# Kernel tuning notes

Measured on AMD Instinct MI355X. Metric: run time of the kernel, lower is better.

Reference implementation:

```python
import jax, jax.numpy as jnp
import numpy as np
from jax import lax

EPSILON = 0.05      # sinkhorn entropic regularization (module init arg)
N_SINKHORN = 100    # fixed iteration count (POT default numItermax=1000 w/ early stop 1e-9)


def setup_inputs() -> dict:
    key = jax.random.key(0)
    k1, k2, k3 = jax.random.split(key, 3)
    B, D = 2048, 1024
    audio_emb = jax.random.normal(k1, (B, D), dtype=jnp.float32)
    text_emb = jax.random.normal(k2, (B, D), dtype=jnp.float32)
    # learned metric L (set via set_L); PSD so diag(L) > 0 and sqrt is real
    A = jax.random.normal(k3, (D, D), dtype=jnp.float32)
    L = (A @ A.T) / jnp.float32(D)
    return {"audio_emb": audio_emb, "text_emb": text_emb, "L": L}


def reference(audio_emb, text_emb, L):
    B = audio_emb.shape[0]
    M = jnp.nan_to_num(L)
    # SVD is computed in the original (reg term), but the final loss discards it
    s = jnp.linalg.svd(M, compute_uv=False)
    _reg = jnp.sum(s)  # unused in returned loss (original: loss = wloss)

    # einsum('ijk,ikj,kk->ij') only reads diag(M):
    # M_dist[i,j] = sum_k diag(M)[k] * (audio[j,k] - text[i,k])^2
    w = jnp.diagonal(M)  # [D]
    aw = jnp.einsum('jd,d->j', audio_emb * audio_emb, w)        # [B]
    tw = jnp.einsum('id,d->i', text_emb * text_emb, w)          # [B]
    cross = jnp.einsum('id,jd->ij', text_emb * w, audio_emb)    # [B,B]
    M_dist = tw[:, None] + aw[None, :] - 2.0 * cross
    M_dist = jnp.sqrt(jnp.maximum(M_dist, 0.0))
    M_dist = M_dist / jnp.max(M_dist)

    # Sinkhorn-Knopp (ot.sinkhorn, method='sinkhorn')
    a = jnp.ones((B,), dtype=M_dist.dtype) / B
    b = jnp.ones((B,), dtype=M_dist.dtype) / B
    K = jnp.exp(-M_dist / EPSILON)  # [B,B]

    def step(uv, _):
        u, v = uv
        v = b / (K.T @ u)
        u = a / (K @ v)
        return (u, v), None

    u0 = jnp.ones((B,), dtype=M_dist.dtype) / B
    v0 = jnp.ones((B,), dtype=M_dist.dtype) / B
    (u, v), _ = lax.scan(step, (u0, v0), None, length=N_SINKHORN)
    # pi = diag(u) K diag(v); pi_hat = eye(B)/B -> only diag(pi) matters
    pi_diag = u * jnp.diagonal(K) * v  # [B]
    wloss = -jnp.sum(jnp.log(pi_diag)) / B
    return wloss
```

## Files before the change

### kernel.cpp

```cpp
#include <hip/hip_runtime.h>
#include <hip/hip_fp16.h>
#include <math.h>

#define NB 2048
#define ND 1024
#define EPS 0.05f
#define NITER 100
#define SBLK 256

typedef float f32x4 __attribute__((ext_vector_type(4)));
typedef float f32x2 __attribute__((ext_vector_type(2)));
typedef short s16x8 __attribute__((ext_vector_type(8)));
typedef unsigned short u16x4 __attribute__((ext_vector_type(4)));
union Uh { f32x4 f; __half2 h[4]; };

__global__ void prep_k(const float* __restrict__ L, float* __restrict__ w,
                       float* __restrict__ u, float* __restrict__ v,
                       unsigned* __restrict__ maxbits, unsigned* __restrict__ flags) {
    int gtid = blockIdx.x * 256 + threadIdx.x;
    if (gtid < ND) {
        float x = L[(size_t)gtid * (ND + 1)];
        if (x != x) x = 0.f;
        else if (fabsf(x) == INFINITY) x = (x > 0.f) ? 3.4028235e38f : -3.4028235e38f;
        w[gtid] = x;
    }
    u[gtid] = 1.0f / NB;
    v[gtid] = 1.0f / NB;
    if (gtid == 0) *maxbits = 0u;
    if (gtid < 1024) flags[gtid] = 0u;
}

__global__ __launch_bounds__(256) void rows_k(const float* __restrict__ audio,
                                              const float* __restrict__ text,
                                              const float* __restrict__ w,
                                              float* __restrict__ aw, float* __restrict__ tw) {
    int r = blockIdx.x, tid = threadIdx.x;
    float4 wv = *(const float4*)&w[tid * 4];
    float4 a4 = *(const float4*)&audio[(size_t)r * ND + tid * 4];
    float4 t4 = *(const float4*)&text[(size_t)r * ND + tid * 4];
    float sa = a4.x * a4.x * wv.x + a4.y * a4.y * wv.y + a4.z * a4.z * wv.z + a4.w * a4.w * wv.w;
    float st = t4.x * t4.x * wv.x + t4.y * t4.y * wv.y + t4.z * t4.z * wv.z + t4.w * t4.w * wv.w;
    #pragma unroll
    for (int off = 32; off; off >>= 1) {
        sa += __shfl_down(sa, off, 64);
        st += __shfl_down(st, off, 64);
    }
    __shared__ float red[8];
    if ((tid & 63) == 0) { red[tid >> 6] = sa; red[4 + (tid >> 6)] = st; }
    __syncthreads();
    if (tid == 0) {
        aw[r] = red[0] + red[1] + red[2] + red[3];
        tw[r] = red[4] + red[5] + red[6] + red[7];
    }
}

__device__ __forceinline__ unsigned short f2bf(float x) {
    unsigned uu = __float_as_uint(x);
    return (unsigned short)((uu + 0x7FFFu + ((uu >> 16) & 1u)) >> 16);
}

__global__ __launch_bounds__(256) void gemm_mdist(
        const float* __restrict__ Tm, const float* __restrict__ Am,
        const float* __restrict__ wd, const float* __restrict__ tw, const float* __restrict__ aw,
        __half* __restrict__ Md, __half* __restrict__ MdT,
        float* __restrict__ diagMd, unsigned* __restrict__ maxbits) {
    __shared__ __align__(16) unsigned char smem[38912];
    float* wl = (float*)(smem + 34816);
    const int t = threadIdx.x;
    const int row0 = blockIdx.y * 128, col0 = blockIdx.x * 128;
    *(f32x4*)&wl[t * 4] = *(const f32x4*)&wd[t * 4];
    const int wv = t >> 6;
    const int wr = wv >> 1, wc = wv & 1;
    const int l = t & 63, lr = l & 15, kg = l >> 4;
    const int trow = t >> 4, tk4 = t & 15;
    const int px = (((tk4 >> 1) ^ (trow & 7)) << 4) + ((tk4 & 1) << 3);
    f32x4 acc[4][4];
    #pragma unroll
    for (int m = 0; m < 4; ++m)
        #pragma unroll
        for (int n = 0; n < 4; ++n) acc[m][n] = (f32x4){0.f, 0.f, 0.f, 0.f};
    __syncthreads();
    const float* tp = Tm + (size_t)(row0 + trow) * ND + tk4 * 4;
    const float* ap = Am + (size_t)(col0 + trow) * ND + tk4 * 4;
    for (int k0 = 0; k0 < ND; k0 += 64) {
        f32x4 wv4 = *(const f32x4*)&wl[k0 + tk4 * 4];
        __syncthreads();
        #pragma unroll
        for (int s = 0; s < 8; ++s) {
            f32x4 tv = *(const f32x4*)(tp + (size_t)(s * 16) * ND + k0);
            f32x4 av = *(const f32x4*)(ap + (size_t)(s * 16) * ND + k0);
            tv *= wv4;
            u16x4 tb, ab;
            tb[0] = f2bf(tv[0]); tb[1] = f2bf(tv[1]); tb[2] = f2bf(tv[2]); tb[3] = f2bf(tv[3]);
            ab[0] = f2bf(av[0]); ab[1] = f2bf(av[1]); ab[2] = f2bf(av[2]); ab[3] = f2bf(av[3]);
            const int rb = (s * 16 + trow) * 128 + px;
            *(u16x4*)(smem + rb) = tb;
            *(u16x4*)(smem + 16384 + rb) = ab;
        }
        __syncthreads();
        #pragma unroll
        for (int kk = 0; kk < 2; ++kk) {
            const int sl = (((kk << 2) + kg) ^ (lr & 7)) << 4;
            s16x8 af[4], bfr[4];
            #pragma unroll
            for (int m = 0; m < 4; ++m)
                af[m] = *(const s16x8*)(smem + (wr * 64 + m * 16 + lr) * 128 + sl);
            #pragma unroll
            for (int n = 0; n < 4; ++n)
                bfr[n] = *(const s16x8*)(smem + 16384 + (wc * 64 + n * 16 + lr) * 128 + sl);
            #pragma unroll
            for (int m = 0; m < 4; ++m)
                #pragma unroll
                for (int n = 0; n < 4; ++n)
                    acc[m][n] = __builtin_amdgcn_mfma_f32_16x16x32_bf16(af[m], bfr[n], acc[m][n], 0, 0, 0);
        }
    }
    __syncthreads();
    unsigned short* tr = (unsigned short*)smem;
    unsigned short* mdp = (unsigned short*)Md;
    float lmax = 0.f;
    #pragma unroll
    for (int m = 0; m < 4; ++m) {
        #pragma unroll
        for (int r = 0; r < 4; ++r) {
            const int li = wr * 64 + m * 16 + kg * 4 + r;
            const int i = row0 + li;
            const float twi = tw[i];
            #pragma unroll
            for (int n = 0; n < 4; ++n) {
                const int lj = wc * 64 + n * 16 + lr;
                const int j = col0 + lj;
                float md = twi + aw[j] - 2.0f * acc[m][n][r];
                md = sqrtf(fmaxf(md, 0.f));
                lmax = fmaxf(lmax, md);
                const unsigned short hb = __half_as_ushort(__float2half(md));
                mdp[(size_t)i * NB + j] = hb;
                tr[lj * 136 + li] = hb;
                if (i == j) diagMd[i] = md;
            }
        }
    }
    __syncthreads();
    {
        const int jj = t >> 1, ih = (t & 1) * 64;
        unsigned short* dst = (unsigned short*)MdT + (size_t)(col0 + jj) * NB + row0 + ih;
        #pragma unroll
        for (int x = 0; x < 8; ++x)
            *(s16x8*)(dst + x * 8) = *(const s16x8*)&tr[jj * 136 + ih + x * 8];
    }
    #pragma unroll
    for (int off = 32; off; off >>= 1) lmax = fmaxf(lmax, __shfl_down(lmax, off, 64));
    float* red = (float*)(smem + 34816);
    if (l == 0) red[t >> 6] = lmax;
    __syncthreads();
    if (t == 0) {
        float m2 = fmaxf(fmaxf(red[0], red[1]), fmaxf(red[2], red[3]));
        atomicMax(maxbits, __float_as_uint(m2));
    }
}

__device__ __forceinline__ void wait_phase(const unsigned* __restrict__ flags, int l,
                                           unsigned ph) {
    const unsigned* p = flags + (l << 2);
    for (;;) {
        unsigned f0, f1, f2, f3;
        asm volatile("global_load_dword %0, %4, off sc0 sc1\n\t"
                     "global_load_dword %1, %5, off sc0 sc1\n\t"
                     "global_load_dword %2, %6, off sc0 sc1\n\t"
                     "global_load_dword %3, %7, off sc0 sc1\n\t"
                     "s_waitcnt vmcnt(0)"
                     : "=&v"(f0), "=&v"(f1), "=&v"(f2), "=&v"(f3)
                     : "v"(p), "v"(p + 256), "v"(p + 512), "v"(p + 768) : "memory");
        if (__all((f0 >= ph) && (f1 >= ph) && (f2 >= ph) && (f3 >= ph))) break;
        __builtin_amdgcn_s_sleep(1);
    }
}

__device__ __forceinline__ void half_step_reg(const f32x4 (&kreg)[2][8],
                                              const float* __restrict__ xin,
                                              float* __restrict__ xout,
                                              int row0, float ab, int l) {
    const float* p0 = xin + (l << 3);
    f32x4 x[8];
    asm volatile("global_load_dwordx4 %0, %8, off sc0 sc1\n\t"
                 "global_load_dwordx4 %1, %9, off sc0 sc1\n\t"
                 "global_load_dwordx4 %2, %10, off sc0 sc1\n\t"
                 "global_load_dwordx4 %3, %11, off sc0 sc1\n\t"
                 "global_load_dwordx4 %4, %12, off sc0 sc1\n\t"
                 "global_load_dwordx4 %5, %13, off sc0 sc1\n\t"
                 "global_load_dwordx4 %6, %14, off sc0 sc1\n\t"
                 "global_load_dwordx4 %7, %15, off sc0 sc1\n\t"
                 "s_waitcnt vmcnt(0)"
                 : "=&v"(x[0]), "=&v"(x[1]), "=&v"(x[2]), "=&v"(x[3]),
                   "=&v"(x[4]), "=&v"(x[5]), "=&v"(x[6]), "=&v"(x[7])
                 : "v"(p0), "v"(p0 + 4), "v"(p0 + 512), "v"(p0 + 516),
                   "v"(p0 + 1024), "v"(p0 + 1028), "v"(p0 + 1536), "v"(p0 + 1540)
                 : "memory");
    float acc0 = 0.f, acc1 = 0.f;
    #pragma unroll
    for (int j = 0; j < 8; ++j) {
        #pragma unroll
        for (int q = 0; q < 4; ++q) {
            acc0 = fmaf(kreg[0][j][q], x[j][q], acc0);
            acc1 = fmaf(kreg[1][j][q], x[j][q], acc1);
        }
    }
    #pragma unroll
    for (int off = 32; off; off >>= 1) {
        acc0 += __shfl_down(acc0, off, 64);
        acc1 += __shfl_down(acc1, off, 64);
    }
    if (l == 0) {
        f32x2 o;
        o[0] = ab / acc0; o[1] = ab / acc1;
        asm volatile("global_store_dwordx2 %1, %0, off sc0 sc1"
                     :: "v"(o), "v"(xout + row0) : "memory");
    }
    asm volatile("s_waitcnt vmcnt(0)" ::: "memory");
}

__global__ __launch_bounds__(256, 1) void sinkhorn_k(
        const __half* __restrict__ Mdr, const __half* __restrict__ Mdc,
        float* __restrict__ u, float* __restrict__ v,
        const unsigned* __restrict__ maxbits, unsigned* __restrict__ flags) {
    const int tid = threadIdx.x, bid = blockIdx.x;
    const int w = tid >> 6, l = tid & 63;
    const int row0 = (bid << 3) + (w << 1);
    const float ab = 1.0f / NB;
    unsigned* myflag = flags + (bid << 2);
    const float mx = __uint_as_float(*maxbits);
    const float cc = -1.0f / (mx * EPS);
    f32x4 kc[2][8], kr[2][8];
    #pragma unroll
    for (int r = 0; r < 2; ++r) {
        const __half* pc = Mdc + (size_t)(row0 + r) * NB;
        const __half* pr = Mdr + (size_t)(row0 + r) * NB;
        #pragma unroll
        for (int c = 0; c < 4; ++c) {
            const int col = (c << 9) + (l << 3);
            Uh a; a.f = *(const f32x4*)(pc + col);
            Uh b; b.f = *(const f32x4*)(pr + col);
            #pragma unroll
            for (int q = 0; q < 4; ++q) {
                float2 fa = __half22float2(a.h[q]);
                float2 fb = __half22float2(b.h[q]);
                kc[r][2 * c + (q >> 1)][(q & 1) * 2]     = __expf(fa.x * cc);
                kc[r][2 * c + (q >> 1)][(q & 1) * 2 + 1] = __expf(fa.y * cc);
                kr[r][2 * c + (q >> 1)][(q & 1) * 2]     = __expf(fb.x * cc);
                kr[r][2 * c + (q >> 1)][(q & 1) * 2 + 1] = __expf(fb.y * cc);
            }
        }
    }
    for (int it = 0; it < NITER; ++it) {
        wait_phase(flags, l, 2 * it);
        half_step_reg(kc, u, v, row0, ab, l);
        __syncthreads();
        if (tid == 0) {
            unsigned ph = 2 * it + 1;
            asm volatile("global_store_dword %1, %0, off sc0 sc1"
                         :: "v"(ph), "v"(myflag) : "memory");
        }
        wait_phase(flags, l, 2 * it + 1);
        half_step_reg(kr, v, u, row0, ab, l);
        __syncthreads();
        if (tid == 0) {
            unsigned ph = 2 * it + 2;
            asm volatile("global_store_dword %1, %0, off sc0 sc1"
                         :: "v"(ph), "v"(myflag) : "memory");
        }
    }
}

__global__ void loss_k(const float* __restrict__ u, const float* __restrict__ v,
                       const float* __restrict__ diagMd, const unsigned* __restrict__ maxbits,
                       float* __restrict__ out) {
    int tid = threadIdx.x;
    float mx = __uint_as_float(*maxbits);
    float cc = 1.0f / (mx * EPS);
    double s = 0.0;
    for (int i = tid; i < NB; i += 256)
        s += (double)(logf(u[i]) + logf(v[i]) - diagMd[i] * cc);
    #pragma unroll
    for (int off = 32; off; off >>= 1) s += __shfl_down(s, off, 64);
    __shared__ double red[4];
    if ((tid & 63) == 0) red[tid >> 6] = s;
    __syncthreads();
    if (tid == 0)
        out[0] = (float)(-(red[0] + red[1] + red[2] + red[3]) / (double)NB);
}

extern "C" void kernel_launch(void* const* d_in, const int* in_sizes, int n_in,
                              void* d_out, int out_size, void* d_ws, size_t ws_size,
                              hipStream_t stream) {
    const float* audio = (const float*)d_in[0];
    const float* text  = (const float*)d_in[1];
    const float* L     = (const float*)d_in[2];
    char* ws = (char*)d_ws;
    float*    w       = (float*)(ws + 0);
    float*    aw      = (float*)(ws + 4096);
    float*    tw      = (float*)(ws + 12288);
    float*    u       = (float*)(ws + 20480);
    float*    v       = (float*)(ws + 28672);
    float*    diagMd  = (float*)(ws + 36864);
    unsigned* maxbits = (unsigned*)(ws + 45056);
    unsigned* flags   = (unsigned*)(ws + 45312);
    __half*   Md      = (__half*)(ws + 65536);
    __half*   MdT     = (__half*)(ws + 65536 + (size_t)NB * NB * 2);

    prep_k<<<8, 256, 0, stream>>>(L, w, u, v, maxbits, flags);
    rows_k<<<NB, 256, 0, stream>>>(audio, text, w, aw, tw);
    gemm_mdist<<<dim3(16, 16), 256, 0, stream>>>(text, audio, w, tw, aw, Md, MdT, diagMd, maxbits);
    sinkhorn_k<<<SBLK, 256, 0, stream>>>(Md, MdT, u, v, maxbits, flags);
    loss_k<<<1, 256, 0, stream>>>(u, v, diagMd, maxbits, (float*)d_out);
}
```

Measured before the change: 713.8 us.

## Replace flag barrier with epoch-tagged bf16 vector entries in Sinkhorn

Each u/v entry is packed with a 16-bit epoch tag and a bf16 value, so consumers poll the data itself instead of polling separate per-block flags and then reloading the vector. This removes the __syncthreads, the flag store and the extra round trip per half-step, and it makes the column mapping contiguous for each lane. In exchange u/v carry only bf16 precision, which adds rounding error to the Sinkhorn iterations and the loss. Correctness now depends on the tag and value being written atomically within a single 32-bit store.

```diff
diff --git a/kernel.cpp b/kernel.cpp
--- a/kernel.cpp
+++ b/kernel.cpp
@@ -9,14 +9,20 @@
 #define SBLK 256
 
 typedef float f32x4 __attribute__((ext_vector_type(4)));
-typedef float f32x2 __attribute__((ext_vector_type(2)));
+typedef unsigned u32x4 __attribute__((ext_vector_type(4)));
+typedef unsigned u32x2 __attribute__((ext_vector_type(2)));
 typedef short s16x8 __attribute__((ext_vector_type(8)));
 typedef unsigned short u16x4 __attribute__((ext_vector_type(4)));
 union Uh { f32x4 f; __half2 h[4]; };
 
+__device__ __forceinline__ unsigned short f2bf(float x) {
+    unsigned uu = __float_as_uint(x);
+    return (unsigned short)((uu + 0x7FFFu + ((uu >> 16) & 1u)) >> 16);
+}
+
 __global__ void prep_k(const float* __restrict__ L, float* __restrict__ w,
-                       float* __restrict__ u, float* __restrict__ v,
-                       unsigned* __restrict__ maxbits, unsigned* __restrict__ flags) {
+                       unsigned* __restrict__ uP, unsigned* __restrict__ vP,
+                       unsigned* __restrict__ maxbits) {
     int gtid = blockIdx.x * 256 + threadIdx.x;
     if (gtid < ND) {
         float x = L[(size_t)gtid * (ND + 1)];
@@ -24,10 +30,9 @@
         else if (fabsf(x) == INFINITY) x = (x > 0.f) ? 3.4028235e38f : -3.4028235e38f;
         w[gtid] = x;
     }
-    u[gtid] = 1.0f / NB;
-    v[gtid] = 1.0f / NB;
+    uP[gtid] = 0x3A00u;
+    vP[gtid] = 0x3A00u;
     if (gtid == 0) *maxbits = 0u;
-    if (gtid < 1024) flags[gtid] = 0u;
 }
 
 __global__ __launch_bounds__(256) void rows_k(const float* __restrict__ audio,
@@ -52,11 +57,6 @@
         aw[r] = red[0] + red[1] + red[2] + red[3];
         tw[r] = red[4] + red[5] + red[6] + red[7];
     }
-}
-
-__device__ __forceinline__ unsigned short f2bf(float x) {
-    unsigned uu = __float_as_uint(x);
-    return (unsigned short)((uu + 0x7FFFu + ((uu >> 16) & 1u)) >> 16);
 }
 
 __global__ __launch_bounds__(256) void gemm_mdist(
@@ -159,50 +159,50 @@
     }
 }
 
-__device__ __forceinline__ void wait_phase(const unsigned* __restrict__ flags, int l,
-                                           unsigned ph) {
-    const unsigned* p = flags + (l << 2);
-    for (;;) {
-        unsigned f0, f1, f2, f3;
-        asm volatile("global_load_dword %0, %4, off sc0 sc1\n\t"
-                     "global_load_dword %1, %5, off sc0 sc1\n\t"
-                     "global_load_dword %2, %6, off sc0 sc1\n\t"
-                     "global_load_dword %3, %7, off sc0 sc1\n\t"
-                     "s_waitcnt vmcnt(0)"
-                     : "=&v"(f0), "=&v"(f1), "=&v"(f2), "=&v"(f3)
-                     : "v"(p), "v"(p + 256), "v"(p + 512), "v"(p + 768) : "memory");
-        if (__all((f0 >= ph) && (f1 >= ph) && (f2 >= ph) && (f3 >= ph))) break;
+#define LOAD8(p0) asm volatile( \
+        "global_load_dwordx4 %0, %8, off sc0 sc1\n\t" \
+        "global_load_dwordx4 %1, %8, off offset:16 sc0 sc1\n\t" \
+        "global_load_dwordx4 %2, %8, off offset:32 sc0 sc1\n\t" \
+        "global_load_dwordx4 %3, %8, off offset:48 sc0 sc1\n\t" \
+        "global_load_dwordx4 %4, %8, off offset:64 sc0 sc1\n\t" \
+        "global_load_dwordx4 %5, %8, off offset:80 sc0 sc1\n\t" \
+        "global_load_dwordx4 %6, %8, off offset:96 sc0 sc1\n\t" \
+        "global_load_dwordx4 %7, %8, off offset:112 sc0 sc1\n\t" \
+        "s_waitcnt vmcnt(0)" \
+        : "=&v"(d0), "=&v"(d1), "=&v"(d2), "=&v"(d3), \
+          "=&v"(d4), "=&v"(d5), "=&v"(d6), "=&v"(d7) \
+        : "v"(p0) : "memory")
+
+#define CHK4(dd) ((dd[0] >= phw) && (dd[1] >= phw) && (dd[2] >= phw) && (dd[3] >= phw))
+
+__device__ __forceinline__ void half_step_pair(const f32x4 (&kreg)[2][8],
+                                               const unsigned* __restrict__ xin,
+                                               unsigned* __restrict__ xout,
+                                               int row0, float ab, int l,
+                                               unsigned ph, unsigned epout) {
+    const unsigned phw = ph << 16;
+    const unsigned* p0 = xin + (l << 5);
+    u32x4 d0, d1, d2, d3, d4, d5, d6, d7;
+    LOAD8(p0);
+    bool ok = CHK4(d0) && CHK4(d1) && CHK4(d2) && CHK4(d3) &&
+              CHK4(d4) && CHK4(d5) && CHK4(d6) && CHK4(d7);
+    while (!__all(ok)) {
         __builtin_amdgcn_s_sleep(1);
-    }
-}
-
-__device__ __forceinline__ void half_step_reg(const f32x4 (&kreg)[2][8],
-                                              const float* __restrict__ xin,
-                                              float* __restrict__ xout,
-                                              int row0, float ab, int l) {
-    const float* p0 = xin + (l << 3);
-    f32x4 x[8];
-    asm volatile("global_load_dwordx4 %0, %8, off sc0 sc1\n\t"
-                 "global_load_dwordx4 %1, %9, off sc0 sc1\n\t"
-                 "global_load_dwordx4 %2, %10, off sc0 sc1\n\t"
-                 "global_load_dwordx4 %3, %11, off sc0 sc1\n\t"
-                 "global_load_dwordx4 %4, %12, off sc0 sc1\n\t"
-                 "global_load_dwordx4 %5, %13, off sc0 sc1\n\t"
-                 "global_load_dwordx4 %6, %14, off sc0 sc1\n\t"
-                 "global_load_dwordx4 %7, %15, off sc0 sc1\n\t"
-                 "s_waitcnt vmcnt(0)"
-                 : "=&v"(x[0]), "=&v"(x[1]), "=&v"(x[2]), "=&v"(x[3]),
-                   "=&v"(x[4]), "=&v"(x[5]), "=&v"(x[6]), "=&v"(x[7])
-                 : "v"(p0), "v"(p0 + 4), "v"(p0 + 512), "v"(p0 + 516),
-                   "v"(p0 + 1024), "v"(p0 + 1028), "v"(p0 + 1536), "v"(p0 + 1540)
-                 : "memory");
+        if (!ok) {
+            LOAD8(p0);
+            ok = CHK4(d0) && CHK4(d1) && CHK4(d2) && CHK4(d3) &&
+                 CHK4(d4) && CHK4(d5) && CHK4(d6) && CHK4(d7);
+        }
+    }
+    const u32x4 dd[8] = {d0, d1, d2, d3, d4, d5, d6, d7};
     float acc0 = 0.f, acc1 = 0.f;
     #pragma unroll
     for (int j = 0; j < 8; ++j) {
         #pragma unroll
-        for (int q = 0; q < 4; ++q) {
-            acc0 = fmaf(kreg[0][j][q], x[j][q], acc0);
-            acc1 = fmaf(kreg[1][j][q], x[j][q], acc1);
+        for (int k = 0; k < 4; ++k) {
+            float xv = __uint_as_float(dd[j][k] << 16);
+            acc0 = fmaf(kreg[0][j][k], xv, acc0);
+            acc1 = fmaf(kreg[1][j][k], xv, acc1);
         }
     }
     #pragma unroll
@@ -211,75 +211,63 @@
         acc1 += __shfl_down(acc1, off, 64);
     }
     if (l == 0) {
-        f32x2 o;
-        o[0] = ab / acc0; o[1] = ab / acc1;
+        const unsigned tag = epout << 16;
+        u32x2 o;
+        o[0] = tag | (unsigned)f2bf(ab / acc0);
+        o[1] = tag | (unsigned)f2bf(ab / acc1);
         asm volatile("global_store_dwordx2 %1, %0, off sc0 sc1"
                      :: "v"(o), "v"(xout + row0) : "memory");
     }
-    asm volatile("s_waitcnt vmcnt(0)" ::: "memory");
 }
 
 __global__ __launch_bounds__(256, 1) void sinkhorn_k(
         const __half* __restrict__ Mdr, const __half* __restrict__ Mdc,
-        float* __restrict__ u, float* __restrict__ v,
-        const unsigned* __restrict__ maxbits, unsigned* __restrict__ flags) {
+        unsigned* __restrict__ uP, unsigned* __restrict__ vP,
+        const unsigned* __restrict__ maxbits) {
     const int tid = threadIdx.x, bid = blockIdx.x;
     const int w = tid >> 6, l = tid & 63;
     const int row0 = (bid << 3) + (w << 1);
     const float ab = 1.0f / NB;
-    unsigned* myflag = flags + (bid << 2);
     const float mx = __uint_as_float(*maxbits);
     const float cc = -1.0f / (mx * EPS);
     f32x4 kc[2][8], kr[2][8];
     #pragma unroll
     for (int r = 0; r < 2; ++r) {
-        const __half* pc = Mdc + (size_t)(row0 + r) * NB;
-        const __half* pr = Mdr + (size_t)(row0 + r) * NB;
-        #pragma unroll
-        for (int c = 0; c < 4; ++c) {
-            const int col = (c << 9) + (l << 3);
-            Uh a; a.f = *(const f32x4*)(pc + col);
-            Uh b; b.f = *(const f32x4*)(pr + col);
-            #pragma unroll
-            for (int q = 0; q < 4; ++q) {
-                float2 fa = __half22float2(a.h[q]);
-                float2 fb = __half22float2(b.h[q]);
-                kc[r][2 * c + (q >> 1)][(q & 1) * 2]     = __expf(fa.x * cc);
-                kc[r][2 * c + (q >> 1)][(q & 1) * 2 + 1] = __expf(fa.y * cc);
-                kr[r][2 * c + (q >> 1)][(q & 1) * 2]     = __expf(fb.x * cc);
-                kr[r][2 * c + (q >> 1)][(q & 1) * 2 + 1] = __expf(fb.y * cc);
+        const __half* pc = Mdc + (size_t)(row0 + r) * NB + (l << 5);
+        const __half* pr = Mdr + (size_t)(row0 + r) * NB + (l << 5);
+        #pragma unroll
+        for (int q = 0; q < 4; ++q) {
+            Uh a; a.f = *(const f32x4*)(pc + (q << 3));
+            Uh b; b.f = *(const f32x4*)(pr + (q << 3));
+            #pragma unroll
+            for (int h = 0; h < 4; ++h) {
+                float2 fa = __half22float2(a.h[h]);
+                float2 fb = __half22float2(b.h[h]);
+                kc[r][2 * q + (h >> 1)][(h & 1) * 2]     = __expf(fa.x * cc);
+                kc[r][2 * q + (h >> 1)][(h & 1) * 2 + 1] = __expf(fa.y * cc);
+                kr[r][2 * q + (h >> 1)][(h & 1) * 2]     = __expf(fb.x * cc);
+                kr[r][2 * q + (h >> 1)][(h & 1) * 2 + 1] = __expf(fb.y * cc);
             }
         }
     }
-    for (int it = 0; it < NITER; ++it) {
-        wait_phase(flags, l, 2 * it);
-        half_step_reg(kc, u, v, row0, ab, l);
-        __syncthreads();
-        if (tid == 0) {
-            unsigned ph = 2 * it + 1;
-            asm volatile("global_store_dword %1, %0, off sc0 sc1"
-                         :: "v"(ph), "v"(myflag) : "memory");
-        }
-        wait_phase(flags, l, 2 * it + 1);
-        half_step_reg(kr, v, u, row0, ab, l);
-        __syncthreads();
-        if (tid == 0) {
-            unsigned ph = 2 * it + 2;
-            asm volatile("global_store_dword %1, %0, off sc0 sc1"
-                         :: "v"(ph), "v"(myflag) : "memory");
-        }
-    }
-}
-
-__global__ void loss_k(const float* __restrict__ u, const float* __restrict__ v,
+    for (unsigned it = 0; it < NITER; ++it) {
+        half_step_pair(kc, uP, vP, row0, ab, l, it, it + 1);
+        half_step_pair(kr, vP, uP, row0, ab, l, it + 1, it + 1);
+    }
+}
+
+__global__ void loss_k(const unsigned* __restrict__ uP, const unsigned* __restrict__ vP,
                        const float* __restrict__ diagMd, const unsigned* __restrict__ maxbits,
                        float* __restrict__ out) {
     int tid = threadIdx.x;
     float mx = __uint_as_float(*maxbits);
     float cc = 1.0f / (mx * EPS);
     double s = 0.0;
-    for (int i = tid; i < NB; i += 256)
-        s += (double)(logf(u[i]) + logf(v[i]) - diagMd[i] * cc);
+    for (int i = tid; i < NB; i += 256) {
+        float ui = __uint_as_float(uP[i] << 16);
+        float vi = __uint_as_float(vP[i] << 16);
+        s += (double)(logf(ui) + logf(vi) - diagMd[i] * cc);
+    }
     #pragma unroll
     for (int off = 32; off; off >>= 1) s += __shfl_down(s, off, 64);
     __shared__ double red[4];
@@ -299,17 +287,16 @@
     float*    w       = (float*)(ws + 0);
     float*    aw      = (float*)(ws + 4096);
     float*    tw      = (float*)(ws + 12288);
-    float*    u       = (float*)(ws + 20480);
-    float*    v       = (float*)(ws + 28672);
+    unsigned* uP      = (unsigned*)(ws + 20480);
+    unsigned* vP      = (unsigned*)(ws + 28672);
     float*    diagMd  = (float*)(ws + 36864);
     unsigned* maxbits = (unsigned*)(ws + 45056);
-    unsigned* flags   = (unsigned*)(ws + 45312);
     __half*   Md      = (__half*)(ws + 65536);
     __half*   MdT     = (__half*)(ws + 65536 + (size_t)NB * NB * 2);
 
-    prep_k<<<8, 256, 0, stream>>>(L, w, u, v, maxbits, flags);
+    prep_k<<<8, 256, 0, stream>>>(L, w, uP, vP, maxbits);
     rows_k<<<NB, 256, 0, stream>>>(audio, text, w, aw, tw);
     gemm_mdist<<<dim3(16, 16), 256, 0, stream>>>(text, audio, w, tw, aw, Md, MdT, diagMd, maxbits);
-    sinkhorn_k<<<SBLK, 256, 0, stream>>>(Md, MdT, u, v, maxbits, flags);
-    loss_k<<<1, 256, 0, stream>>>(u, v, diagMd, maxbits, (float*)d_out);
-}
+    sinkhorn_k<<<SBLK, 256, 0, stream>>>(Md, MdT, uP, vP, maxbits);
+    loss_k<<<1, 256, 0, stream>>>(uP, vP, diagMd, maxbits, (float*)d_out);
+}
```

After: 2.298 ms. 3.22x slower.

## Use per-wavefront phase flags in Sinkhorn grid barrier instead of block sync

Applied to the files above, without the earlier changes.

Each wavefront now publishes its own phase flag immediately after storing its two outputs, which removes the block-level __syncthreads and the per-block flag store. The poll loop reads all 1024 wave flags with four dwordx4 loads per lane instead of four scalar dword loads. This shortens the critical path of the cross-block barrier that runs 200 times, at the cost of each wave polling four times as many flag words per load.

```diff
diff --git a/kernel.cpp b/kernel.cpp
--- a/kernel.cpp
+++ b/kernel.cpp
@@ -10,9 +10,15 @@
 
 typedef float f32x4 __attribute__((ext_vector_type(4)));
 typedef float f32x2 __attribute__((ext_vector_type(2)));
+typedef unsigned u32x4 __attribute__((ext_vector_type(4)));
 typedef short s16x8 __attribute__((ext_vector_type(8)));
 typedef unsigned short u16x4 __attribute__((ext_vector_type(4)));
 union Uh { f32x4 f; __half2 h[4]; };
+
+__device__ __forceinline__ unsigned f2bf(float x) {
+    unsigned uu = __float_as_uint(x);
+    return (uu + 0x7FFFu + ((uu >> 16) & 1u)) >> 16;
+}
 
 __global__ void prep_k(const float* __restrict__ L, float* __restrict__ w,
                        float* __restrict__ u, float* __restrict__ v,
@@ -52,11 +58,6 @@
         aw[r] = red[0] + red[1] + red[2] + red[3];
         tw[r] = red[4] + red[5] + red[6] + red[7];
     }
-}
-
-__device__ __forceinline__ unsigned short f2bf(float x) {
-    unsigned uu = __float_as_uint(x);
-    return (unsigned short)((uu + 0x7FFFu + ((uu >> 16) & 1u)) >> 16);
 }
 
 __global__ __launch_bounds__(256) void gemm_mdist(
@@ -91,8 +92,10 @@
             f32x4 av = *(const f32x4*)(ap + (size_t)(s * 16) * ND + k0);
             tv *= wv4;
             u16x4 tb, ab;
-            tb[0] = f2bf(tv[0]); tb[1] = f2bf(tv[1]); tb[2] = f2bf(tv[2]); tb[3] = f2bf(tv[3]);
-            ab[0] = f2bf(av[0]); ab[1] = f2bf(av[1]); ab[2] = f2bf(av[2]); ab[3] = f2bf(av[3]);
+            tb[0] = (unsigned short)f2bf(tv[0]); tb[1] = (unsigned short)f2bf(tv[1]);
+            tb[2] = (unsigned short)f2bf(tv[2]); tb[3] = (unsigned short)f2bf(tv[3]);
+            ab[0] = (unsigned short)f2bf(av[0]); ab[1] = (unsigned short)f2bf(av[1]);
+            ab[2] = (unsigned short)f2bf(av[2]); ab[3] = (unsigned short)f2bf(av[3]);
             const int rb = (s * 16 + trow) * 128 + px;
             *(u16x4*)(smem + rb) = tb;
             *(u16x4*)(smem + 16384 + rb) = ab;
@@ -159,19 +162,21 @@
     }
 }
 
+#define CHK4(dd) ((dd[0] >= ph) && (dd[1] >= ph) && (dd[2] >= ph) && (dd[3] >= ph))
+
 __device__ __forceinline__ void wait_phase(const unsigned* __restrict__ flags, int l,
                                            unsigned ph) {
     const unsigned* p = flags + (l << 2);
     for (;;) {
-        unsigned f0, f1, f2, f3;
-        asm volatile("global_load_dword %0, %4, off sc0 sc1\n\t"
-                     "global_load_dword %1, %5, off sc0 sc1\n\t"
-                     "global_load_dword %2, %6, off sc0 sc1\n\t"
-                     "global_load_dword %3, %7, off sc0 sc1\n\t"
+        u32x4 d0, d1, d2, d3;
+        asm volatile("global_load_dwordx4 %0, %4, off sc0 sc1\n\t"
+                     "global_load_dwordx4 %1, %4, off offset:1024 sc0 sc1\n\t"
+                     "global_load_dwordx4 %2, %4, off offset:2048 sc0 sc1\n\t"
+                     "global_load_dwordx4 %3, %4, off offset:3072 sc0 sc1\n\t"
                      "s_waitcnt vmcnt(0)"
-                     : "=&v"(f0), "=&v"(f1), "=&v"(f2), "=&v"(f3)
-                     : "v"(p), "v"(p + 256), "v"(p + 512), "v"(p + 768) : "memory");
-        if (__all((f0 >= ph) && (f1 >= ph) && (f2 >= ph) && (f3 >= ph))) break;
+                     : "=&v"(d0), "=&v"(d1), "=&v"(d2), "=&v"(d3)
+                     : "v"(p) : "memory");
+        if (__all(CHK4(d0) && CHK4(d1) && CHK4(d2) && CHK4(d3))) break;
         __builtin_amdgcn_s_sleep(1);
     }
 }
@@ -179,7 +184,8 @@
 __device__ __forceinline__ void half_step_reg(const f32x4 (&kreg)[2][8],
                                               const float* __restrict__ xin,
                                               float* __restrict__ xout,
-                                              int row0, float ab, int l) {
+                                              int row0, float ab, int l,
+                                              unsigned* __restrict__ flagp, unsigned ph) {
     const float* p0 = xin + (l << 3);
     f32x4 x[8];
     asm volatile("global_load_dwordx4 %0, %8, off sc0 sc1\n\t"
@@ -213,10 +219,11 @@
     if (l == 0) {
         f32x2 o;
         o[0] = ab / acc0; o[1] = ab / acc1;
-        asm volatile("global_store_dwordx2 %1, %0, off sc0 sc1"
-                     :: "v"(o), "v"(xout + row0) : "memory");
-    }
-    asm volatile("s_waitcnt vmcnt(0)" ::: "memory");
+        asm volatile("global_store_dwordx2 %1, %0, off sc0 sc1\n\t"
+                     "s_waitcnt vmcnt(0)\n\t"
+                     "global_store_dword %3, %2, off sc0 sc1"
+                     :: "v"(o), "v"(xout + row0), "v"(ph), "v"(flagp) : "memory");
+    }
 }
 
 __global__ __launch_bounds__(256, 1) void sinkhorn_k(
@@ -227,7 +234,7 @@
     const int w = tid >> 6, l = tid & 63;
     const int row0 = (bid << 3) + (w << 1);
     const float ab = 1.0f / NB;
-    unsigned* myflag = flags + (bid << 2);
+    unsigned* myflag = flags + (bid << 2) + w;
     const float mx = __uint_as_float(*maxbits);
     const float cc = -1.0f / (mx * EPS);
     f32x4 kc[2][8], kr[2][8];
@@ -253,21 +260,9 @@
     }
     for (int it = 0; it < NITER; ++it) {
         wait_phase(flags, l, 2 * it);
-        half_step_reg(kc, u, v, row0, ab, l);
-        __syncthreads();
-        if (tid == 0) {
-            unsigned ph = 2 * it + 1;
-            asm volatile("global_store_dword %1, %0, off sc0 sc1"
-                         :: "v"(ph), "v"(myflag) : "memory");
-        }
+        half_step_reg(kc, u, v, row0, ab, l, myflag, 2 * it + 1);
         wait_phase(flags, l, 2 * it + 1);
-        half_step_reg(kr, v, u, row0, ab, l);
-        __syncthreads();
-        if (tid == 0) {
-            unsigned ph = 2 * it + 2;
-            asm volatile("global_store_dword %1, %0, off sc0 sc1"
-                         :: "v"(ph), "v"(myflag) : "memory");
-        }
+        half_step_reg(kr, v, u, row0, ab, l, myflag, 2 * it + 2);
     }
 }
 
```

New measurement: 1.800 ms. 152% more time.
